# Performance work log

Measured on AMD Instinct MI355X. Metric: run time of the kernel, lower is better.

Reference implementation:

```python
import jax, jax.numpy as jnp
import numpy as np

B, L, H, NH, NB = 16, 200, 128, 2, 2
ITEMS, SPAN = 50000, 256
NEG = -2.0**32 + 1.0  # mask value used by the torch module


def _ln(x, g, b, eps=1e-8):
    m = jnp.mean(x, axis=-1, keepdims=True)
    v = jnp.mean((x - m) ** 2, axis=-1, keepdims=True)
    return (x - m) / jnp.sqrt(v + eps) * g + b


def setup_inputs() -> dict:
    key = jax.random.key(0)
    ks = jax.random.split(key, 20)
    p = lambda k, s: (jax.random.normal(k, s, jnp.float32) * 0.02)
    item_emb = p(ks[0], (ITEMS + 1, H)).at[0].set(0.0)  # padding_idx=0
    return {
        "user_ids": jax.random.randint(ks[1], (B,), 0, 10000),
        "log_seqs": jax.random.randint(ks[2], (B, L), 0, ITEMS),
        "time_matrices": jax.random.randint(ks[3], (B, L, L), 0, SPAN),
        "pos_seqs": jax.random.randint(ks[4], (B, L), 0, ITEMS),
        "neg_seqs": jax.random.randint(ks[5], (B, L), 0, ITEMS),
        "item_emb": item_emb,
        "pos_K_emb": p(ks[6], (L, H)),
        "pos_V_emb": p(ks[7], (L, H)),
        "time_K_emb": p(ks[8], (SPAN + 1, H)),
        "time_V_emb": p(ks[9], (SPAN + 1, H)),
        "Wq": p(ks[10], (NB, H, H)), "bq": jnp.zeros((NB, H)),
        "Wk": p(ks[11], (NB, H, H)), "bk": jnp.zeros((NB, H)),
        "Wv": p(ks[12], (NB, H, H)), "bv": jnp.zeros((NB, H)),
        "ln1_g": jnp.ones((NB, H)), "ln1_b": jnp.zeros((NB, H)),
        "W1": p(ks[13], (NB, H, H)), "b1": jnp.zeros((NB, H)),
        "W2": p(ks[14], (NB, H, H)), "b2": jnp.zeros((NB, H)),
        "ln2_g": jnp.ones((NB, H)), "ln2_b": jnp.zeros((NB, H)),
        "lnf_g": jnp.ones((H,)), "lnf_b": jnp.zeros((H,)),
    }


def reference(user_ids, log_seqs, time_matrices, pos_seqs, neg_seqs,
              item_emb, pos_K_emb, pos_V_emb, time_K_emb, time_V_emb,
              Wq, bq, Wk, bk, Wv, bv, ln1_g, ln1_b,
              W1, b1, W2, b2, ln2_g, ln2_b, lnf_g, lnf_b):
    d = H // NH
    pad = (log_seqs == 0)                    # (B,L) timeline mask
    keep = (~pad)[..., None].astype(jnp.float32)

    seqs = item_emb[log_seqs] * jnp.sqrt(jnp.float32(H))
    seqs = seqs * keep
    posK = pos_K_emb.reshape(L, NH, d)       # same for every batch element
    posV = pos_V_emb.reshape(L, NH, d)
    tmK = time_K_emb[time_matrices].reshape(B, L, L, NH, d)  # (B,L,L,h,d)
    tmV = time_V_emb[time_matrices].reshape(B, L, L, NH, d)
    causal = ~jnp.tril(jnp.ones((L, L), dtype=bool))          # True = masked
    mask = pad[:, None, :, None] | causal[None, None, :, :]   # (B,1,L,L) row-mask | causal

    for i in range(NB):
        Q = (seqs @ Wq[i].T + bq[i]).reshape(B, L, NH, d)
        K = (seqs @ Wk[i].T + bk[i]).reshape(B, L, NH, d)
        V = (seqs @ Wv[i].T + bv[i]).reshape(B, L, NH, d)
        aw = jnp.einsum('bqhd,bkhd->bhqk', Q, K)
        aw = aw + jnp.einsum('bqhd,khd->bhqk', Q, posK)
        aw = aw + jnp.einsum('bqkhd,bqhd->bhqk', tmK, Q)
        aw = aw / jnp.sqrt(jnp.float32(d))
        aw = jnp.where(mask, NEG, aw)
        A = jax.nn.softmax(aw, axis=-1)                        # (B,h,L,L)
        out = jnp.einsum('bhqk,bkhd->bqhd', A, V)
        out = out + jnp.einsum('bhqk,khd->bqhd', A, posV)
        out = out + jnp.einsum('bhqk,bqkhd->bqhd', A, tmV)
        out = out.reshape(B, L, H)
        seqs = _ln(seqs + out, ln1_g[i], ln1_b[i])
        ffn = jax.nn.relu(seqs @ W1[i].T + b1[i]) @ W2[i].T + b2[i]
        seqs = _ln(seqs + ffn, ln2_g[i], ln2_b[i])
        seqs = seqs * keep

    log_feats = _ln(seqs, lnf_g, lnf_b)
    pos_logits = jnp.sum(log_feats * item_emb[pos_seqs], axis=-1)  # (B,L)
    neg_logits = jnp.sum(log_feats * item_emb[neg_seqs], axis=-1)
    return jnp.stack([pos_logits, neg_logits])  # (2,B,L)
```

## Files before the change

### kernel.cpp

```cpp
#include <hip/hip_runtime.h>
#include <hip/hip_bf16.h>
#include <math.h>

#define BB 16
#define LL 200
#define HH 128
#define DD 64
#define NQT 25
#define NEGF -4294967295.0f
#define SQRTH 11.313708498984761f

__global__ __launch_bounds__(512) void k_qkv(float* __restrict__ seqs,
    const int* __restrict__ log_seqs, const float* __restrict__ item_emb,
    const float* __restrict__ Wq, const float* __restrict__ bq,
    const float* __restrict__ Wk, const float* __restrict__ bk,
    const float* __restrict__ Wv, const float* __restrict__ bv,
    const float* __restrict__ posK, const float* __restrict__ posV,
    float* __restrict__ Q, float* __restrict__ Kp, float* __restrict__ Vp) {
    __shared__ float s_lds[16][HH];
    int r0g = blockIdx.x * 16;
    int t = threadIdx.x;
    {
        int r = t >> 5, d4 = t & 31;
        int id = log_seqs[r0g + r];
        float4 v = make_float4(0.f, 0.f, 0.f, 0.f);
        if (id != 0) {
            v = ((const float4*)(item_emb + id * HH))[d4];
            v.x *= SQRTH; v.y *= SQRTH; v.z *= SQRTH; v.w *= SQRTH;
        }
        *(float4*)&s_lds[r][d4 * 4] = v;
        ((float4*)(seqs + r0g * HH))[t] = v;
    }
    __syncthreads();
    int c = t & 127, rg = t >> 7;
    float aq[4] = {0.f, 0.f, 0.f, 0.f};
    float ak[4] = {0.f, 0.f, 0.f, 0.f};
    float av[4] = {0.f, 0.f, 0.f, 0.f};
    const float4* wq4 = (const float4*)(Wq + c * HH);
    const float4* wk4 = (const float4*)(Wk + c * HH);
    const float4* wv4 = (const float4*)(Wv + c * HH);
#pragma unroll 4
    for (int k4 = 0; k4 < HH / 4; ++k4) {
        float4 wq = wq4[k4], wk = wk4[k4], wv = wv4[k4];
#pragma unroll
        for (int r = 0; r < 4; ++r) {
            float4 s = *(const float4*)&s_lds[rg * 4 + r][k4 * 4];
            aq[r] += s.x * wq.x + s.y * wq.y + s.z * wq.z + s.w * wq.w;
            ak[r] += s.x * wk.x + s.y * wk.y + s.z * wk.z + s.w * wk.w;
            av[r] += s.x * wv.x + s.y * wv.y + s.z * wv.z + s.w * wv.w;
        }
    }
#pragma unroll
    for (int r = 0; r < 4; ++r) {
        int row = r0g + rg * 4 + r;
        int l = row % LL;
        Q[row * HH + c]  = aq[r] + bq[c];
        Kp[row * HH + c] = ak[r] + bk[c] + posK[l * HH + c];
        Vp[row * HH + c] = av[r] + bv[c] + posV[l * HH + c];
    }
}

__global__ __launch_bounds__(256) void k_proj(const float* __restrict__ Q,
    const float* __restrict__ timeK, float* __restrict__ projK) {
    int bh = blockIdx.x / 25, qt = blockIdx.x % 25;
    int b = bh >> 1, h = bh & 1;
    int qlo = qt * 8;
    __shared__ float Qs[8][68];
    __shared__ float TK[32][68];
    int t = threadIdx.x;
    if (t < 128) {
        int r = t >> 4, d4 = t & 15;
        *(float4*)&Qs[r][d4 * 4] =
            ((const float4*)(Q + (b * LL + qlo + r) * HH + h * DD))[d4];
    }
    int tq = t >> 5, ttl = t & 31;
    for (int ch = 0; ch < 9; ++ch) {
        int base = ch * 32;
        __syncthreads();
        for (int x = t; x < 512; x += 256) {
            int i = x >> 4, d4 = x & 15;
            int tt = base + i;
            if (tt < 257)
                *(float4*)&TK[i][d4 * 4] =
                    ((const float4*)(timeK + tt * HH + h * DD))[d4];
        }
        __syncthreads();
        int tt = base + ttl;
        if (tt < 257) {
            float acc = 0.f;
#pragma unroll
            for (int d4 = 0; d4 < 16; ++d4) {
                float4 qv = *(const float4*)&Qs[tq][d4 * 4];
                float4 kv = *(const float4*)&TK[ttl][d4 * 4];
                acc += qv.x * kv.x + qv.y * kv.y + qv.z * kv.z + qv.w * kv.w;
            }
            projK[(bh * LL + qlo + tq) * 257 + tt] = acc;
        }
    }
}

__global__ __launch_bounds__(256) void k_attn(
    const float* __restrict__ Q, const float* __restrict__ Kp, const float* __restrict__ Vp,
    const float* __restrict__ projK, const float* __restrict__ timeV,
    const int* __restrict__ tm, const int* __restrict__ log_seqs,
    float* __restrict__ attnout) {
    int bh = blockIdx.x / NQT, qt = blockIdx.x % NQT;
    int b = bh >> 1, h = bh & 1;
    int qlo = qt * 8;
    __shared__ float K_s[32][68];
    __shared__ float smemW[457 * 12];
    __shared__ int s_allmask;
#define WT(i, j) smemW[(i) * 12 + (j)]
    int t = threadIdx.x;
    int tq = t >> 5, lane = t & 31, g = tq;
    int q = qlo + tq;
    int qhi = qlo + 7;

    if (t == 0) s_allmask = 0;
    for (int x = 200 * 12 + t; x < 457 * 12; x += 256) smemW[x] = 0.f;
    float4 qreg[16];
    {
        const float4* qp = (const float4*)(Q + (b * LL + q) * HH + h * DD);
#pragma unroll
        for (int d4 = 0; d4 < 16; ++d4) qreg[d4] = qp[d4];
    }
    const int* tmrow = tm + (b * LL + q) * LL;
    const float* projrow = projK + (bh * LL + q) * 257;
    const int* lsrow = log_seqs + b * LL;

    float s[7];
#pragma unroll
    for (int j = 0; j < 7; ++j) s[j] = NEGF;
    int nkc = (qhi >> 5) + 1;
#pragma unroll
    for (int kc = 0; kc < 7; ++kc) {
        if (kc < nkc) {
            int kbase = kc * 32;
            for (int x = t; x < 512; x += 256) {
                int i = x >> 4, d4 = x & 15;
                int k = kbase + i;
                if (k < LL)
                    *(float4*)&K_s[i][d4 * 4] =
                        ((const float4*)(Kp + (b * LL + k) * HH + h * DD))[d4];
            }
            __syncthreads();
            int k = kbase + lane;
            if (k <= q && lsrow[k] != 0) {
                float acc = 0.f;
#pragma unroll
                for (int d4 = 0; d4 < 16; ++d4) {
                    float4 kv = *(const float4*)&K_s[lane][d4 * 4];
                    acc += qreg[d4].x * kv.x + qreg[d4].y * kv.y +
                           qreg[d4].z * kv.z + qreg[d4].w * kv.w;
                }
                s[kc] = (acc + projrow[tmrow[k]]) * 0.125f;
            }
            __syncthreads();
        }
    }

    float mx = s[0];
#pragma unroll
    for (int j = 1; j < 7; ++j) mx = fmaxf(mx, s[j]);
    mx = fmaxf(mx, __shfl_xor(mx, 1, 64));
    mx = fmaxf(mx, __shfl_xor(mx, 2, 64));
    mx = fmaxf(mx, __shfl_xor(mx, 4, 64));
    mx = fmaxf(mx, __shfl_xor(mx, 8, 64));
    mx = fmaxf(mx, __shfl_xor(mx, 16, 64));
    bool allmask = (mx == NEGF);
    float sum = 0.f;
#pragma unroll
    for (int j = 0; j < 7; ++j) {
        int k = lane + 32 * j;
        float e = (k < LL) ? __expf(s[j] - mx) : 0.f;
        s[j] = e;
        sum += e;
    }
    sum += __shfl_xor(sum, 1, 64);
    sum += __shfl_xor(sum, 2, 64);
    sum += __shfl_xor(sum, 4, 64);
    sum += __shfl_xor(sum, 8, 64);
    sum += __shfl_xor(sum, 16, 64);
    float inv = 1.0f / sum;
    int klim = allmask ? LL : (q + 1);
    if (allmask && lane == 0) s_allmask = 1;
#pragma unroll
    for (int j = 0; j < 7; ++j) {
        int k = lane + 32 * j;
        if (k < LL) {
            float p = s[j] * inv;
            WT(k, tq) = p;
            if (k < klim && p != 0.f)
                atomicAdd(&WT(200 + tmrow[k], tq), p);
        }
    }
    __syncthreads();

    int kmax = s_allmask ? LL : (qhi + 1);
    float a00=0.f,a01=0.f,a10=0.f,a11=0.f,a20=0.f,a21=0.f,a30=0.f,a31=0.f;
    float a40=0.f,a41=0.f,a50=0.f,a51=0.f,a60=0.f,a61=0.f,a70=0.f,a71=0.f;
#define PV_STEP(WROW, SRCPTR)                                            \
    {                                                                    \
        const float* wr = &WROW;                                         \
        float4 w0 = *(const float4*)wr;                                  \
        float4 w1 = *(const float4*)(wr + 4);                            \
        float2 vv = *(const float2*)(SRCPTR);                            \
        a00 += w0.x * vv.x; a01 += w0.x * vv.y;                          \
        a10 += w0.y * vv.x; a11 += w0.y * vv.y;                          \
        a20 += w0.z * vv.x; a21 += w0.z * vv.y;                          \
        a30 += w0.w * vv.x; a31 += w0.w * vv.y;                          \
        a40 += w1.x * vv.x; a41 += w1.x * vv.y;                          \
        a50 += w1.y * vv.x; a51 += w1.y * vv.y;                          \
        a60 += w1.z * vv.x; a61 += w1.z * vv.y;                          \
        a70 += w1.w * vv.x; a71 += w1.w * vv.y;                          \
    }
    for (int i = g; i < kmax; i += 8)
        PV_STEP(WT(i, 0), Vp + (b * LL + i) * HH + h * DD + lane * 2);
    for (int i = g; i < 257; i += 8)
        PV_STEP(WT(200 + i, 0), timeV + i * HH + h * DD + lane * 2);
#undef PV_STEP
    __syncthreads();
    float* part = smemW;
    part[g * 512 + 0 * 64 + lane * 2] = a00; part[g * 512 + 0 * 64 + lane * 2 + 1] = a01;
    part[g * 512 + 1 * 64 + lane * 2] = a10; part[g * 512 + 1 * 64 + lane * 2 + 1] = a11;
    part[g * 512 + 2 * 64 + lane * 2] = a20; part[g * 512 + 2 * 64 + lane * 2 + 1] = a21;
    part[g * 512 + 3 * 64 + lane * 2] = a30; part[g * 512 + 3 * 64 + lane * 2 + 1] = a31;
    part[g * 512 + 4 * 64 + lane * 2] = a40; part[g * 512 + 4 * 64 + lane * 2 + 1] = a41;
    part[g * 512 + 5 * 64 + lane * 2] = a50; part[g * 512 + 5 * 64 + lane * 2 + 1] = a51;
    part[g * 512 + 6 * 64 + lane * 2] = a60; part[g * 512 + 6 * 64 + lane * 2 + 1] = a61;
    part[g * 512 + 7 * 64 + lane * 2] = a70; part[g * 512 + 7 * 64 + lane * 2 + 1] = a71;
    __syncthreads();
    {
        float ox = 0.f, oy = 0.f;
#pragma unroll
        for (int gg = 0; gg < 8; ++gg) {
            ox += part[gg * 512 + tq * 64 + lane * 2];
            oy += part[gg * 512 + tq * 64 + lane * 2 + 1];
        }
        *(float2*)(attnout + (b * LL + q) * HH + h * DD + lane * 2) =
            make_float2(ox, oy);
    }
#undef WT
}

__global__ __launch_bounds__(512) void k_ffn_full(
    float* __restrict__ seqs, const float* __restrict__ AO,
    const float* __restrict__ g1, const float* __restrict__ be1,
    const float* __restrict__ W1, const float* __restrict__ b1,
    const float* __restrict__ W2, const float* __restrict__ b2,
    const float* __restrict__ g2, const float* __restrict__ be2,
    const int* __restrict__ log_seqs,
    int do_qkv,
    const float* __restrict__ Wq, const float* __restrict__ bq,
    const float* __restrict__ Wk, const float* __restrict__ bk,
    const float* __restrict__ Wv, const float* __restrict__ bv,
    const float* __restrict__ posK, const float* __restrict__ posV,
    float* __restrict__ Q, float* __restrict__ Kp, float* __restrict__ Vp,
    int do_final,
    const float* __restrict__ lnf_g, const float* __restrict__ lnf_b,
    const float* __restrict__ item_emb,
    const int* __restrict__ pos_seqs, const int* __restrict__ neg_seqs,
    float* __restrict__ out) {
    __shared__ float s_lds[16][HH];
    __shared__ float h_lds[16][HH];
    int r0g = blockIdx.x * 16;
    int t = threadIdx.x;
    {
        float4 a = ((const float4*)(seqs + r0g * HH))[t];
        float4 o = ((const float4*)(AO + r0g * HH))[t];
        a.x += o.x; a.y += o.y; a.z += o.z; a.w += o.w;
        ((float4*)s_lds)[t] = a;
    }
    __syncthreads();
    int w = t >> 6, lane = t & 63;
    int lrow = w * 2 + (lane >> 5), cl = lane & 31;
    {
        float sm = 0.f;
#pragma unroll
        for (int j = 0; j < 4; ++j) sm += s_lds[lrow][cl + 32 * j];
        sm += __shfl_xor(sm, 1, 64);  sm += __shfl_xor(sm, 2, 64);
        sm += __shfl_xor(sm, 4, 64);  sm += __shfl_xor(sm, 8, 64);
        sm += __shfl_xor(sm, 16, 64);
        float mean = sm * (1.0f / HH);
        float vr = 0.f;
#pragma unroll
        for (int j = 0; j < 4; ++j) {
            float d = s_lds[lrow][cl + 32 * j] - mean;
            vr += d * d;
        }
        vr += __shfl_xor(vr, 1, 64);  vr += __shfl_xor(vr, 2, 64);
        vr += __shfl_xor(vr, 4, 64);  vr += __shfl_xor(vr, 8, 64);
        vr += __shfl_xor(vr, 16, 64);
        float rstd = rsqrtf(vr * (1.0f / HH) + 1e-8f);
#pragma unroll
        for (int j = 0; j < 4; ++j) {
            int c = cl + 32 * j;
            s_lds[lrow][c] = (s_lds[lrow][c] - mean) * rstd * g1[c] + be1[c];
        }
    }
    __syncthreads();
    int c = t & 127, rg = t >> 7;
    float acc[4] = {0.f, 0.f, 0.f, 0.f};
    const float4* w14 = (const float4*)(W1 + c * HH);
#pragma unroll 4
    for (int k4 = 0; k4 < HH / 4; ++k4) {
        float4 ww = w14[k4];
#pragma unroll
        for (int r = 0; r < 4; ++r) {
            float4 s = *(const float4*)&s_lds[rg * 4 + r][k4 * 4];
            acc[r] += s.x * ww.x + s.y * ww.y + s.z * ww.z + s.w * ww.w;
        }
    }
#pragma unroll
    for (int r = 0; r < 4; ++r) h_lds[rg * 4 + r][c] = fmaxf(acc[r] + b1[c], 0.f);
    __syncthreads();
#pragma unroll
    for (int r = 0; r < 4; ++r) acc[r] = 0.f;
    const float4* w24 = (const float4*)(W2 + c * HH);
#pragma unroll 4
    for (int k4 = 0; k4 < HH / 4; ++k4) {
        float4 ww = w24[k4];
#pragma unroll
        for (int r = 0; r < 4; ++r) {
            float4 s = *(const float4*)&h_lds[rg * 4 + r][k4 * 4];
            acc[r] += s.x * ww.x + s.y * ww.y + s.z * ww.z + s.w * ww.w;
        }
    }
    __syncthreads();
#pragma unroll
    for (int r = 0; r < 4; ++r)
        h_lds[rg * 4 + r][c] = s_lds[rg * 4 + r][c] + acc[r] + b2[c];
    __syncthreads();
    {
        float sm = 0.f;
#pragma unroll
        for (int j = 0; j < 4; ++j) sm += h_lds[lrow][cl + 32 * j];
        sm += __shfl_xor(sm, 1, 64);  sm += __shfl_xor(sm, 2, 64);
        sm += __shfl_xor(sm, 4, 64);  sm += __shfl_xor(sm, 8, 64);
        sm += __shfl_xor(sm, 16, 64);
        float mean = sm * (1.0f / HH);
        float vr = 0.f;
#pragma unroll
        for (int j = 0; j < 4; ++j) {
            float d = h_lds[lrow][cl + 32 * j] - mean;
            vr += d * d;
        }
        vr += __shfl_xor(vr, 1, 64);  vr += __shfl_xor(vr, 2, 64);
        vr += __shfl_xor(vr, 4, 64);  vr += __shfl_xor(vr, 8, 64);
        vr += __shfl_xor(vr, 16, 64);
        float rstd = rsqrtf(vr * (1.0f / HH) + 1e-8f);
        int row = r0g + lrow;
        float keep = (log_seqs[row] != 0) ? 1.0f : 0.0f;
        float y2[4];
#pragma unroll
        for (int j = 0; j < 4; ++j) {
            int cc = cl + 32 * j;
            y2[j] = ((h_lds[lrow][cc] - mean) * rstd * g2[cc] + be2[cc]) * keep;
        }
        if (do_final) {
            float sm2 = y2[0] + y2[1] + y2[2] + y2[3];
            sm2 += __shfl_xor(sm2, 1, 64);  sm2 += __shfl_xor(sm2, 2, 64);
            sm2 += __shfl_xor(sm2, 4, 64);  sm2 += __shfl_xor(sm2, 8, 64);
            sm2 += __shfl_xor(sm2, 16, 64);
            float mean2 = sm2 * (1.0f / HH);
            float vr2 = 0.f;
#pragma unroll
            for (int j = 0; j < 4; ++j) {
                float d = y2[j] - mean2;
                vr2 += d * d;
            }
            vr2 += __shfl_xor(vr2, 1, 64);  vr2 += __shfl_xor(vr2, 2, 64);
            vr2 += __shfl_xor(vr2, 4, 64);  vr2 += __shfl_xor(vr2, 8, 64);
            vr2 += __shfl_xor(vr2, 16, 64);
            float rstd2 = rsqrtf(vr2 * (1.0f / HH) + 1e-8f);
            int pid = pos_seqs[row];
            int nid = neg_seqs[row];
            float pp = 0.f, nn = 0.f;
#pragma unroll
            for (int j = 0; j < 4; ++j) {
                int cc = cl + 32 * j;
                float lf = (y2[j] - mean2) * rstd2 * lnf_g[cc] + lnf_b[cc];
                pp += lf * item_emb[pid * HH + cc];
                nn += lf * item_emb[nid * HH + cc];
            }
            pp += __shfl_xor(pp, 1, 64);  pp += __shfl_xor(pp, 2, 64);
            pp += __shfl_xor(pp, 4, 64);  pp += __shfl_xor(pp, 8, 64);
            pp += __shfl_xor(pp, 16, 64);
            nn += __shfl_xor(nn, 1, 64);  nn += __shfl_xor(nn, 2, 64);
            nn += __shfl_xor(nn, 4, 64);  nn += __shfl_xor(nn, 8, 64);
            nn += __shfl_xor(nn, 16, 64);
            if (cl == 0) {
                out[row] = pp;
                out[BB * LL + row] = nn;
            }
        } else {
#pragma unroll
            for (int j = 0; j < 4; ++j)
                seqs[row * HH + cl + 32 * j] = y2[j];
            if (do_qkv) {
#pragma unroll
                for (int j = 0; j < 4; ++j)
                    s_lds[lrow][cl + 32 * j] = y2[j];
            }
        }
    }
    if (!do_qkv) return;
    __syncthreads();
    float aq[4] = {0.f, 0.f, 0.f, 0.f};
    float ak[4] = {0.f, 0.f, 0.f, 0.f};
    float av[4] = {0.f, 0.f, 0.f, 0.f};
    const float4* wq4 = (const float4*)(Wq + c * HH);
    const float4* wk4 = (const float4*)(Wk + c * HH);
    const float4* wv4 = (const float4*)(Wv + c * HH);
#pragma unroll 4
    for (int k4 = 0; k4 < HH / 4; ++k4) {
        float4 wq = wq4[k4], wk = wk4[k4], wv = wv4[k4];
#pragma unroll
        for (int r = 0; r < 4; ++r) {
            float4 s = *(const float4*)&s_lds[rg * 4 + r][k4 * 4];
            aq[r] += s.x * wq.x + s.y * wq.y + s.z * wq.z + s.w * wq.w;
            ak[r] += s.x * wk.x + s.y * wk.y + s.z * wk.z + s.w * wk.w;
            av[r] += s.x * wv.x + s.y * wv.y + s.z * wv.z + s.w * wv.w;
        }
    }
#pragma unroll
    for (int r = 0; r < 4; ++r) {
        int row = r0g + rg * 4 + r;
        int l = row % LL;
        Q[row * HH + c]  = aq[r] + bq[c];
        Kp[row * HH + c] = ak[r] + bk[c] + posK[l * HH + c];
        Vp[row * HH + c] = av[r] + bv[c] + posV[l * HH + c];
    }
}

extern "C" void kernel_launch(void* const* d_in, const int* in_sizes, int n_in,
                              void* d_out, int out_size, void* d_ws, size_t ws_size,
                              hipStream_t stream) {
    const int* log_seqs = (const int*)d_in[1];
    const int* tm       = (const int*)d_in[2];
    const int* pos_seqs = (const int*)d_in[3];
    const int* neg_seqs = (const int*)d_in[4];
    const float* item_emb = (const float*)d_in[5];
    const float* posK   = (const float*)d_in[6];
    const float* posV   = (const float*)d_in[7];
    const float* timeK  = (const float*)d_in[8];
    const float* timeV  = (const float*)d_in[9];
    const float* Wq = (const float*)d_in[10];
    const float* bq = (const float*)d_in[11];
    const float* Wk = (const float*)d_in[12];
    const float* bk = (const float*)d_in[13];
    const float* Wv = (const float*)d_in[14];
    const float* bv = (const float*)d_in[15];
    const float* ln1_g = (const float*)d_in[16];
    const float* ln1_b = (const float*)d_in[17];
    const float* W1 = (const float*)d_in[18];
    const float* b1 = (const float*)d_in[19];
    const float* W2 = (const float*)d_in[20];
    const float* b2 = (const float*)d_in[21];
    const float* ln2_g = (const float*)d_in[22];
    const float* ln2_b = (const float*)d_in[23];
    const float* lnf_g = (const float*)d_in[24];
    const float* lnf_b = (const float*)d_in[25];

    float* ws    = (float*)d_ws;
    float* seqs  = ws;
    float* Qb    = seqs + 409600;
    float* Kpb   = Qb + 409600;
    float* Vpb   = Kpb + 409600;
    float* AO    = Vpb + 409600;
    float* projK = AO + 409600;

    k_qkv<<<BB * LL / 16, 512, 0, stream>>>(seqs, log_seqs, item_emb,
        Wq, bq, Wk, bk, Wv, bv, posK, posV, Qb, Kpb, Vpb);
    k_proj<<<32 * NQT, 256, 0, stream>>>(Qb, timeK, projK);
    k_attn<<<32 * NQT, 256, 0, stream>>>(Qb, Kpb, Vpb, projK, timeV,
                                         tm, log_seqs, AO);
    k_ffn_full<<<BB * LL / 16, 512, 0, stream>>>(seqs, AO,
        ln1_g, ln1_b, W1, b1, W2, b2, ln2_g, ln2_b, log_seqs,
        1, Wq + HH * HH, bq + HH, Wk + HH * HH, bk + HH, Wv + HH * HH, bv + HH,
        posK, posV, Qb, Kpb, Vpb,
        0, lnf_g, lnf_b, item_emb, pos_seqs, neg_seqs, (float*)d_out);
    k_proj<<<32 * NQT, 256, 0, stream>>>(Qb, timeK, projK);
    k_attn<<<32 * NQT, 256, 0, stream>>>(Qb, Kpb, Vpb, projK, timeV,
                                         tm, log_seqs, AO);
    k_ffn_full<<<BB * LL / 16, 512, 0, stream>>>(seqs, AO,
        ln1_g + HH, ln1_b + HH, W1 + HH * HH, b1 + HH, W2 + HH * HH, b2 + HH,
        ln2_g + HH, ln2_b + HH, log_seqs,
        0, nullptr, nullptr, nullptr, nullptr, nullptr, nullptr,
        nullptr, nullptr, nullptr, nullptr, nullptr,
        1, lnf_g, lnf_b, item_emb, pos_seqs, neg_seqs, (float*)d_out);
}
```

Before: 183.7 us.

## Double-buffer LDS tiles in proj/attn and unfuse second-block QKV from FFN

k_proj and k_attn now keep two LDS tile buffers. Each prefetches the next timeK/K chunk while computing on the current one, which removes one barrier per chunk. The QKV projection for block 2 is taken out of the FFN kernel, and k_qkv gains a mode that reads seqs from global memory instead of embedding it. This adds a fourth kernel launch and an extra seqs round trip in exchange for a lighter FFN kernel and overlapped loads.

```diff
diff --git a/kernel.cpp b/kernel.cpp
--- a/kernel.cpp
+++ b/kernel.cpp
@@ -11,7 +11,7 @@
 #define SQRTH 11.313708498984761f
 
 __global__ __launch_bounds__(512) void k_qkv(float* __restrict__ seqs,
-    const int* __restrict__ log_seqs, const float* __restrict__ item_emb,
+    const int* __restrict__ log_seqs, const float* __restrict__ item_emb, int do_embed,
     const float* __restrict__ Wq, const float* __restrict__ bq,
     const float* __restrict__ Wk, const float* __restrict__ bk,
     const float* __restrict__ Wv, const float* __restrict__ bv,
@@ -20,7 +20,7 @@
     __shared__ float s_lds[16][HH];
     int r0g = blockIdx.x * 16;
     int t = threadIdx.x;
-    {
+    if (do_embed) {
         int r = t >> 5, d4 = t & 31;
         int id = log_seqs[r0g + r];
         float4 v = make_float4(0.f, 0.f, 0.f, 0.f);
@@ -30,6 +30,8 @@
         }
         *(float4*)&s_lds[r][d4 * 4] = v;
         ((float4*)(seqs + r0g * HH))[t] = v;
+    } else {
+        ((float4*)s_lds)[t] = ((const float4*)(seqs + r0g * HH))[t];
     }
     __syncthreads();
     int c = t & 127, rg = t >> 7;
@@ -66,32 +68,38 @@
     int b = bh >> 1, h = bh & 1;
     int qlo = qt * 8;
     __shared__ float Qs[8][68];
-    __shared__ float TK[32][68];
+    __shared__ float TK[2][32][68];
     int t = threadIdx.x;
     if (t < 128) {
         int r = t >> 4, d4 = t & 15;
         *(float4*)&Qs[r][d4 * 4] =
             ((const float4*)(Q + (b * LL + qlo + r) * HH + h * DD))[d4];
     }
+    for (int x = t; x < 512; x += 256) {
+        int i = x >> 4, d4 = x & 15;
+        *(float4*)&TK[0][i][d4 * 4] =
+            ((const float4*)(timeK + i * HH + h * DD))[d4];
+    }
     int tq = t >> 5, ttl = t & 31;
     for (int ch = 0; ch < 9; ++ch) {
-        int base = ch * 32;
         __syncthreads();
-        for (int x = t; x < 512; x += 256) {
-            int i = x >> 4, d4 = x & 15;
-            int tt = base + i;
-            if (tt < 257)
-                *(float4*)&TK[i][d4 * 4] =
-                    ((const float4*)(timeK + tt * HH + h * DD))[d4];
-        }
-        __syncthreads();
-        int tt = base + ttl;
+        if (ch + 1 < 9) {
+            int nb = (ch + 1) * 32;
+            for (int x = t; x < 512; x += 256) {
+                int i = x >> 4, d4 = x & 15;
+                int tt = nb + i;
+                if (tt < 257)
+                    *(float4*)&TK[(ch + 1) & 1][i][d4 * 4] =
+                        ((const float4*)(timeK + tt * HH + h * DD))[d4];
+            }
+        }
+        int tt = ch * 32 + ttl;
         if (tt < 257) {
             float acc = 0.f;
 #pragma unroll
             for (int d4 = 0; d4 < 16; ++d4) {
                 float4 qv = *(const float4*)&Qs[tq][d4 * 4];
-                float4 kv = *(const float4*)&TK[ttl][d4 * 4];
+                float4 kv = *(const float4*)&TK[ch & 1][ttl][d4 * 4];
                 acc += qv.x * kv.x + qv.y * kv.y + qv.z * kv.z + qv.w * kv.w;
             }
             projK[(bh * LL + qlo + tq) * 257 + tt] = acc;
@@ -107,7 +115,7 @@
     int bh = blockIdx.x / NQT, qt = blockIdx.x % NQT;
     int b = bh >> 1, h = bh & 1;
     int qlo = qt * 8;
-    __shared__ float K_s[32][68];
+    __shared__ float K_s[2][32][68];
     __shared__ float smemW[457 * 12];
     __shared__ int s_allmask;
 #define WT(i, j) smemW[(i) * 12 + (j)]
@@ -128,6 +136,12 @@
     const float* projrow = projK + (bh * LL + q) * 257;
     const int* lsrow = log_seqs + b * LL;
 
+    for (int x = t; x < 512; x += 256) {
+        int i = x >> 4, d4 = x & 15;
+        *(float4*)&K_s[0][i][d4 * 4] =
+            ((const float4*)(Kp + (b * LL + i) * HH + h * DD))[d4];
+    }
+
     float s[7];
 #pragma unroll
     for (int j = 0; j < 7; ++j) s[j] = NEGF;
@@ -135,27 +149,28 @@
 #pragma unroll
     for (int kc = 0; kc < 7; ++kc) {
         if (kc < nkc) {
-            int kbase = kc * 32;
-            for (int x = t; x < 512; x += 256) {
-                int i = x >> 4, d4 = x & 15;
-                int k = kbase + i;
-                if (k < LL)
-                    *(float4*)&K_s[i][d4 * 4] =
-                        ((const float4*)(Kp + (b * LL + k) * HH + h * DD))[d4];
-            }
             __syncthreads();
-            int k = kbase + lane;
+            if (kc + 1 < nkc) {
+                int kb = (kc + 1) * 32;
+                for (int x = t; x < 512; x += 256) {
+                    int i = x >> 4, d4 = x & 15;
+                    int k = kb + i;
+                    if (k < LL)
+                        *(float4*)&K_s[(kc + 1) & 1][i][d4 * 4] =
+                            ((const float4*)(Kp + (b * LL + k) * HH + h * DD))[d4];
+                }
+            }
+            int k = kc * 32 + lane;
             if (k <= q && lsrow[k] != 0) {
                 float acc = 0.f;
 #pragma unroll
                 for (int d4 = 0; d4 < 16; ++d4) {
-                    float4 kv = *(const float4*)&K_s[lane][d4 * 4];
+                    float4 kv = *(const float4*)&K_s[kc & 1][lane][d4 * 4];
                     acc += qreg[d4].x * kv.x + qreg[d4].y * kv.y +
                            qreg[d4].z * kv.z + qreg[d4].w * kv.w;
                 }
                 s[kc] = (acc + projrow[tmrow[k]]) * 0.125f;
             }
-            __syncthreads();
         }
     }
 
@@ -249,14 +264,7 @@
     const float* __restrict__ W1, const float* __restrict__ b1,
     const float* __restrict__ W2, const float* __restrict__ b2,
     const float* __restrict__ g2, const float* __restrict__ be2,
-    const int* __restrict__ log_seqs,
-    int do_qkv,
-    const float* __restrict__ Wq, const float* __restrict__ bq,
-    const float* __restrict__ Wk, const float* __restrict__ bk,
-    const float* __restrict__ Wv, const float* __restrict__ bv,
-    const float* __restrict__ posK, const float* __restrict__ posV,
-    float* __restrict__ Q, float* __restrict__ Kp, float* __restrict__ Vp,
-    int do_final,
+    const int* __restrict__ log_seqs, int do_final,
     const float* __restrict__ lnf_g, const float* __restrict__ lnf_b,
     const float* __restrict__ item_emb,
     const int* __restrict__ pos_seqs, const int* __restrict__ neg_seqs,
@@ -357,7 +365,11 @@
             int cc = cl + 32 * j;
             y2[j] = ((h_lds[lrow][cc] - mean) * rstd * g2[cc] + be2[cc]) * keep;
         }
-        if (do_final) {
+        if (!do_final) {
+#pragma unroll
+            for (int j = 0; j < 4; ++j)
+                seqs[row * HH + cl + 32 * j] = y2[j];
+        } else {
             float sm2 = y2[0] + y2[1] + y2[2] + y2[3];
             sm2 += __shfl_xor(sm2, 1, 64);  sm2 += __shfl_xor(sm2, 2, 64);
             sm2 += __shfl_xor(sm2, 4, 64);  sm2 += __shfl_xor(sm2, 8, 64);
@@ -393,43 +405,7 @@
                 out[row] = pp;
                 out[BB * LL + row] = nn;
             }
-        } else {
-#pragma unroll
-            for (int j = 0; j < 4; ++j)
-                seqs[row * HH + cl + 32 * j] = y2[j];
-            if (do_qkv) {
-#pragma unroll
-                for (int j = 0; j < 4; ++j)
-                    s_lds[lrow][cl + 32 * j] = y2[j];
-            }
-        }
-    }
-    if (!do_qkv) return;
-    __syncthreads();
-    float aq[4] = {0.f, 0.f, 0.f, 0.f};
-    float ak[4] = {0.f, 0.f, 0.f, 0.f};
-    float av[4] = {0.f, 0.f, 0.f, 0.f};
-    const float4* wq4 = (const float4*)(Wq + c * HH);
-    const float4* wk4 = (const float4*)(Wk + c * HH);
-    const float4* wv4 = (const float4*)(Wv + c * HH);
-#pragma unroll 4
-    for (int k4 = 0; k4 < HH / 4; ++k4) {
-        float4 wq = wq4[k4], wk = wk4[k4], wv = wv4[k4];
-#pragma unroll
-        for (int r = 0; r < 4; ++r) {
-            float4 s = *(const float4*)&s_lds[rg * 4 + r][k4 * 4];
-            aq[r] += s.x * wq.x + s.y * wq.y + s.z * wq.z + s.w * wq.w;
-            ak[r] += s.x * wk.x + s.y * wk.y + s.z * wk.z + s.w * wk.w;
-            av[r] += s.x * wv.x + s.y * wv.y + s.z * wv.z + s.w * wv.w;
-        }
-    }
-#pragma unroll
-    for (int r = 0; r < 4; ++r) {
-        int row = r0g + rg * 4 + r;
-        int l = row % LL;
-        Q[row * HH + c]  = aq[r] + bq[c];
-        Kp[row * HH + c] = ak[r] + bk[c] + posK[l * HH + c];
-        Vp[row * HH + c] = av[r] + bv[c] + posV[l * HH + c];
+        }
     }
 }
 
@@ -470,23 +446,22 @@
     float* AO    = Vpb + 409600;
     float* projK = AO + 409600;
 
-    k_qkv<<<BB * LL / 16, 512, 0, stream>>>(seqs, log_seqs, item_emb,
-        Wq, bq, Wk, bk, Wv, bv, posK, posV, Qb, Kpb, Vpb);
-    k_proj<<<32 * NQT, 256, 0, stream>>>(Qb, timeK, projK);
-    k_attn<<<32 * NQT, 256, 0, stream>>>(Qb, Kpb, Vpb, projK, timeV,
-                                         tm, log_seqs, AO);
-    k_ffn_full<<<BB * LL / 16, 512, 0, stream>>>(seqs, AO,
-        ln1_g, ln1_b, W1, b1, W2, b2, ln2_g, ln2_b, log_seqs,
-        1, Wq + HH * HH, bq + HH, Wk + HH * HH, bk + HH, Wv + HH * HH, bv + HH,
-        posK, posV, Qb, Kpb, Vpb,
-        0, lnf_g, lnf_b, item_emb, pos_seqs, neg_seqs, (float*)d_out);
-    k_proj<<<32 * NQT, 256, 0, stream>>>(Qb, timeK, projK);
-    k_attn<<<32 * NQT, 256, 0, stream>>>(Qb, Kpb, Vpb, projK, timeV,
-                                         tm, log_seqs, AO);
-    k_ffn_full<<<BB * LL / 16, 512, 0, stream>>>(seqs, AO,
-        ln1_g + HH, ln1_b + HH, W1 + HH * HH, b1 + HH, W2 + HH * HH, b2 + HH,
-        ln2_g + HH, ln2_b + HH, log_seqs,
-        0, nullptr, nullptr, nullptr, nullptr, nullptr, nullptr,
-        nullptr, nullptr, nullptr, nullptr, nullptr,
-        1, lnf_g, lnf_b, item_emb, pos_seqs, neg_seqs, (float*)d_out);
+    for (int i = 0; i < 2; ++i) {
+        k_qkv<<<BB * LL / 16, 512, 0, stream>>>(seqs, log_seqs, item_emb,
+            (i == 0) ? 1 : 0,
+            Wq + i * HH * HH, bq + i * HH,
+            Wk + i * HH * HH, bk + i * HH,
+            Wv + i * HH * HH, bv + i * HH,
+            posK, posV, Qb, Kpb, Vpb);
+        k_proj<<<32 * NQT, 256, 0, stream>>>(Qb, timeK, projK);
+        k_attn<<<32 * NQT, 256, 0, stream>>>(Qb, Kpb, Vpb, projK, timeV,
+                                             tm, log_seqs, AO);
+        k_ffn_full<<<BB * LL / 16, 512, 0, stream>>>(seqs, AO,
+            ln1_g + i * HH, ln1_b + i * HH,
+            W1 + i * HH * HH, b1 + i * HH,
+            W2 + i * HH * HH, b2 + i * HH,
+            ln2_g + i * HH, ln2_b + i * HH, log_seqs,
+            (i == 1) ? 1 : 0, lnf_g, lnf_b, item_emb,
+            pos_seqs, neg_seqs, (float*)d_out);
+    }
 }
```

After: 186.1 us. No clear change (+1.4%).

## Widen attention query tile to 16 rows with 512-thread blocks

Applied to the files above, without the earlier changes.

The attention kernel now handles 16 queries per block with 512 threads, up from 8 queries with 256 threads. The PV stage is remapped so each thread owns one output column across all 16 queries. Each row of V and timeV loaded from memory therefore serves twice as many queries, and the 257-row timeV sweep is shared by more work. The cost is about half as many blocks (416) on the GPU, a partly wasted final tile with clamped duplicate query rows, and more LDS and registers per block.

```diff
diff --git a/kernel.cpp b/kernel.cpp
--- a/kernel.cpp
+++ b/kernel.cpp
@@ -7,6 +7,7 @@
 #define HH 128
 #define DD 64
 #define NQT 25
+#define NQT16 13
 #define NEGF -4294967295.0f
 #define SQRTH 11.313708498984761f
 
@@ -99,33 +100,34 @@
     }
 }
 
-__global__ __launch_bounds__(256) void k_attn(
+__global__ __launch_bounds__(512) void k_attn(
     const float* __restrict__ Q, const float* __restrict__ Kp, const float* __restrict__ Vp,
     const float* __restrict__ projK, const float* __restrict__ timeV,
     const int* __restrict__ tm, const int* __restrict__ log_seqs,
     float* __restrict__ attnout) {
-    int bh = blockIdx.x / NQT, qt = blockIdx.x % NQT;
+    int bh = blockIdx.x / NQT16, qt = blockIdx.x % NQT16;
     int b = bh >> 1, h = bh & 1;
-    int qlo = qt * 8;
+    int qlo = qt * 16;
     __shared__ float K_s[32][68];
-    __shared__ float smemW[457 * 12];
+    __shared__ float smemW[457 * 24];
     __shared__ int s_allmask;
-#define WT(i, j) smemW[(i) * 12 + (j)]
+#define WT(i, j) smemW[(i) * 24 + (j)]
     int t = threadIdx.x;
-    int tq = t >> 5, lane = t & 31, g = tq;
+    int tq = t >> 5, lane = t & 31;
     int q = qlo + tq;
-    int qhi = qlo + 7;
+    int qq = (q < LL) ? q : (LL - 1);
+    int qhi = qlo + 15; if (qhi > LL - 1) qhi = LL - 1;
 
     if (t == 0) s_allmask = 0;
-    for (int x = 200 * 12 + t; x < 457 * 12; x += 256) smemW[x] = 0.f;
+    for (int x = 200 * 24 + t; x < 457 * 24; x += 512) smemW[x] = 0.f;
     float4 qreg[16];
     {
-        const float4* qp = (const float4*)(Q + (b * LL + q) * HH + h * DD);
+        const float4* qp = (const float4*)(Q + (b * LL + qq) * HH + h * DD);
 #pragma unroll
         for (int d4 = 0; d4 < 16; ++d4) qreg[d4] = qp[d4];
     }
-    const int* tmrow = tm + (b * LL + q) * LL;
-    const float* projrow = projK + (bh * LL + q) * 257;
+    const int* tmrow = tm + (b * LL + qq) * LL;
+    const float* projrow = projK + (bh * LL + qq) * 257;
     const int* lsrow = log_seqs + b * LL;
 
     float s[7];
@@ -136,8 +138,8 @@
     for (int kc = 0; kc < 7; ++kc) {
         if (kc < nkc) {
             int kbase = kc * 32;
-            for (int x = t; x < 512; x += 256) {
-                int i = x >> 4, d4 = x & 15;
+            {
+                int i = t >> 4, d4 = t & 15;
                 int k = kbase + i;
                 if (k < LL)
                     *(float4*)&K_s[i][d4 * 4] =
@@ -145,7 +147,7 @@
             }
             __syncthreads();
             int k = kbase + lane;
-            if (k <= q && lsrow[k] != 0) {
+            if (k <= qq && lsrow[k] != 0) {
                 float acc = 0.f;
 #pragma unroll
                 for (int d4 = 0; d4 < 16; ++d4) {
@@ -182,7 +184,7 @@
     sum += __shfl_xor(sum, 8, 64);
     sum += __shfl_xor(sum, 16, 64);
     float inv = 1.0f / sum;
-    int klim = allmask ? LL : (q + 1);
+    int klim = allmask ? LL : (qq + 1);
     if (allmask && lane == 0) s_allmask = 1;
 #pragma unroll
     for (int j = 0; j < 7; ++j) {
@@ -196,49 +198,50 @@
     }
     __syncthreads();
 
+    int g = t >> 6, l64 = t & 63;
     int kmax = s_allmask ? LL : (qhi + 1);
-    float a00=0.f,a01=0.f,a10=0.f,a11=0.f,a20=0.f,a21=0.f,a30=0.f,a31=0.f;
-    float a40=0.f,a41=0.f,a50=0.f,a51=0.f,a60=0.f,a61=0.f,a70=0.f,a71=0.f;
-#define PV_STEP(WROW, SRCPTR)                                            \
+    float acc[16];
+#pragma unroll
+    for (int qi = 0; qi < 16; ++qi) acc[qi] = 0.f;
+#define PV_STEP(WIDX, SRCPTR)                                            \
     {                                                                    \
-        const float* wr = &WROW;                                         \
+        const float* wr = &WT(WIDX, 0);                                  \
         float4 w0 = *(const float4*)wr;                                  \
         float4 w1 = *(const float4*)(wr + 4);                            \
-        float2 vv = *(const float2*)(SRCPTR);                            \
-        a00 += w0.x * vv.x; a01 += w0.x * vv.y;                          \
-        a10 += w0.y * vv.x; a11 += w0.y * vv.y;                          \
-        a20 += w0.z * vv.x; a21 += w0.z * vv.y;                          \
-        a30 += w0.w * vv.x; a31 += w0.w * vv.y;                          \
-        a40 += w1.x * vv.x; a41 += w1.x * vv.y;                          \
-        a50 += w1.y * vv.x; a51 += w1.y * vv.y;                          \
-        a60 += w1.z * vv.x; a61 += w1.z * vv.y;                          \
-        a70 += w1.w * vv.x; a71 += w1.w * vv.y;                          \
+        float4 w2 = *(const float4*)(wr + 8);                            \
+        float4 w3 = *(const float4*)(wr + 12);                           \
+        float vv = *(SRCPTR);                                            \
+        acc[0] += w0.x * vv;  acc[1] += w0.y * vv;                       \
+        acc[2] += w0.z * vv;  acc[3] += w0.w * vv;                       \
+        acc[4] += w1.x * vv;  acc[5] += w1.y * vv;                       \
+        acc[6] += w1.z * vv;  acc[7] += w1.w * vv;                       \
+        acc[8] += w2.x * vv;  acc[9] += w2.y * vv;                       \
+        acc[10] += w2.z * vv; acc[11] += w2.w * vv;                      \
+        acc[12] += w3.x * vv; acc[13] += w3.y * vv;                      \
+        acc[14] += w3.z * vv; acc[15] += w3.w * vv;                      \
     }
     for (int i = g; i < kmax; i += 8)
-        PV_STEP(WT(i, 0), Vp + (b * LL + i) * HH + h * DD + lane * 2);
+        PV_STEP(i, Vp + (b * LL + i) * HH + h * DD + l64);
     for (int i = g; i < 257; i += 8)
-        PV_STEP(WT(200 + i, 0), timeV + i * HH + h * DD + lane * 2);
+        PV_STEP(200 + i, timeV + i * HH + h * DD + l64);
 #undef PV_STEP
     __syncthreads();
     float* part = smemW;
-    part[g * 512 + 0 * 64 + lane * 2] = a00; part[g * 512 + 0 * 64 + lane * 2 + 1] = a01;
-    part[g * 512 + 1 * 64 + lane * 2] = a10; part[g * 512 + 1 * 64 + lane * 2 + 1] = a11;
-    part[g * 512 + 2 * 64 + lane * 2] = a20; part[g * 512 + 2 * 64 + lane * 2 + 1] = a21;
-    part[g * 512 + 3 * 64 + lane * 2] = a30; part[g * 512 + 3 * 64 + lane * 2 + 1] = a31;
-    part[g * 512 + 4 * 64 + lane * 2] = a40; part[g * 512 + 4 * 64 + lane * 2 + 1] = a41;
-    part[g * 512 + 5 * 64 + lane * 2] = a50; part[g * 512 + 5 * 64 + lane * 2 + 1] = a51;
-    part[g * 512 + 6 * 64 + lane * 2] = a60; part[g * 512 + 6 * 64 + lane * 2 + 1] = a61;
-    part[g * 512 + 7 * 64 + lane * 2] = a70; part[g * 512 + 7 * 64 + lane * 2 + 1] = a71;
-    __syncthreads();
-    {
-        float ox = 0.f, oy = 0.f;
-#pragma unroll
-        for (int gg = 0; gg < 8; ++gg) {
-            ox += part[gg * 512 + tq * 64 + lane * 2];
-            oy += part[gg * 512 + tq * 64 + lane * 2 + 1];
-        }
-        *(float2*)(attnout + (b * LL + q) * HH + h * DD + lane * 2) =
-            make_float2(ox, oy);
+#pragma unroll
+    for (int qi = 0; qi < 16; ++qi)
+        part[g * 1024 + qi * 64 + l64] = acc[qi];
+    __syncthreads();
+    {
+#pragma unroll
+        for (int rep = 0; rep < 2; ++rep) {
+            int idx = t + rep * 512;
+            int q16 = idx >> 6, d = idx & 63;
+            float ox = 0.f;
+#pragma unroll
+            for (int gg = 0; gg < 8; ++gg) ox += part[gg * 1024 + idx];
+            if (qlo + q16 < LL)
+                attnout[(b * LL + qlo + q16) * HH + h * DD + d] = ox;
+        }
     }
 #undef WT
 }
@@ -473,16 +476,16 @@
     k_qkv<<<BB * LL / 16, 512, 0, stream>>>(seqs, log_seqs, item_emb,
         Wq, bq, Wk, bk, Wv, bv, posK, posV, Qb, Kpb, Vpb);
     k_proj<<<32 * NQT, 256, 0, stream>>>(Qb, timeK, projK);
-    k_attn<<<32 * NQT, 256, 0, stream>>>(Qb, Kpb, Vpb, projK, timeV,
-                                         tm, log_seqs, AO);
+    k_attn<<<32 * NQT16, 512, 0, stream>>>(Qb, Kpb, Vpb, projK, timeV,
+                                           tm, log_seqs, AO);
     k_ffn_full<<<BB * LL / 16, 512, 0, stream>>>(seqs, AO,
         ln1_g, ln1_b, W1, b1, W2, b2, ln2_g, ln2_b, log_seqs,
         1, Wq + HH * HH, bq + HH, Wk + HH * HH, bk + HH, Wv + HH * HH, bv + HH,
         posK, posV, Qb, Kpb, Vpb,
         0, lnf_g, lnf_b, item_emb, pos_seqs, neg_seqs, (float*)d_out);
     k_proj<<<32 * NQT, 256, 0, stream>>>(Qb, timeK, projK);
-    k_attn<<<32 * NQT, 256, 0, stream>>>(Qb, Kpb, Vpb, projK, timeV,
-                                         tm, log_seqs, AO);
+    k_attn<<<32 * NQT16, 512, 0, stream>>>(Qb, Kpb, Vpb, projK, timeV,
+                                           tm, log_seqs, AO);
     k_ffn_full<<<BB * LL / 16, 512, 0, stream>>>(seqs, AO,
         ln1_g + HH, ln1_b + HH, W1 + HH * HH, b1 + HH, W2 + HH * HH, b2 + HH,
         ln2_g + HH, ln2_b + HH, log_seqs,
```

Measured after the change: 187.5 us. 1.02x slower.
